# Performance work log

Measured on AMD Instinct MI355X. Metric: run time of the kernel, lower is better.

Reference implementation:

```python
import jax, jax.numpy as jnp
import numpy as np

DIM = 513          # SSP dimension (odd)
N_PARAM = (DIM - 1) // 2
BATCH = 131072


def setup_inputs() -> dict:
    key = jax.random.key(0)
    k1, k2 = jax.random.split(key)
    inputs = jax.random.normal(k1, (BATCH, 1), dtype=jnp.float32)
    # phis initialized uniform in (-pi+0.001, pi-0.001) like the torch module
    phis = jax.random.uniform(k2, (N_PARAM,), dtype=jnp.float32,
                              minval=-np.pi + 0.001, maxval=np.pi - 0.001)
    return {"inputs": inputs, "phis": phis}


def reference(inputs, phis):
    # uf is unit-modulus with conjugate-symmetric spectrum:
    #   uf[0] = 1, uf[1:h] = exp(i*phis), uf[-1:dim//2:-1] = conj(exp(i*phis))
    # so angle(uf) = [0, phis, -phis[::-1]] and uf**x = exp(i * x * angles).
    zero = jnp.zeros((1,), dtype=phis.dtype)
    angles = jnp.concatenate([zero, phis, -phis[::-1]])      # (dim,)
    # inputs: (B, 1) broadcasts against angles (dim,) -> (B, dim)
    spectrum = jnp.exp(1j * (inputs * angles[None, :]).astype(jnp.float32))
    out = jnp.fft.ifft(spectrum, axis=-1).real               # (B, dim)
    return out
```

## Files before the change

kernel.cpp:

```cpp
#include <hip/hip_runtime.h>


#define DIMN 513
#define KDIM 512
#define NPAD 544
#define NPAIRS 17
#define BM 128
#define INV_N (1.0f / 513.0f)

typedef __attribute__((ext_vector_type(8))) short short8;
typedef __attribute__((ext_vector_type(4))) float f32x4;
typedef __attribute__((ext_vector_type(4))) float f4;
typedef __attribute__((ext_vector_type(4), aligned(4))) float f4u;

__device__ __forceinline__ short bf16r(float f) {
  unsigned u = __float_as_uint(f);
  u += 0x7FFFu + ((u >> 16) & 1u);
  return (short)(u >> 16);
}

__global__ void ssp_genB(unsigned short* __restrict__ bt) {
  int idx = blockIdx.x * 256 + threadIdx.x;
  int n = idx >> 9;
  int k = idx & 511;
  int j = k & 255;
  unsigned prod = (unsigned)(j + 1) * (unsigned)n;
  unsigned m = prod % 513u;
  float ang = (float)m * (6.283185307179586f / 513.0f);
  float s, c;
  __sincosf(ang, &s, &c);
  float v = (k < 256) ? c * (2.0f / 513.0f) : -(s * (2.0f / 513.0f));
  unsigned chunk = (unsigned)n >> 5;
  unsigned w = ((unsigned)(n & 31) << 10) + ((unsigned)k << 1);
  unsigned phys = (chunk << 15) + (w ^ ((unsigned)(n & 7) << 4));
  bt[phys >> 1] = (unsigned short)bf16r(v);
}

__global__ __launch_bounds__(256, 2) void ssp_main(
    const float* __restrict__ x, const float* __restrict__ phis,
    const unsigned short* __restrict__ bt, float* __restrict__ out) {
  __shared__ __align__(16) unsigned char lds[65536];
  const int tid = threadIdx.x;
  const int w = tid >> 6;
  const int lane = tid & 63;
  const int r = lane & 15;
  const int q = lane >> 4;
  const long rowW = (long)blockIdx.x * BM + w * 32;

  const unsigned char* btb = (const unsigned char*)bt;

  {
    const unsigned char* src = btb + (w * 8) * 1024 + lane * 16;
    unsigned char* dst = &lds[(w * 8) * 1024];
#pragma unroll
    for (int i = 0; i < 8; ++i)
      __builtin_amdgcn_global_load_lds(
          (const __attribute__((address_space(1))) unsigned int*)(src + i * 1024),
          (__attribute__((address_space(3))) unsigned int*)(dst + i * 1024),
          16, 0, 0);
  }

  short8 afrag[2][16];
  const float x0 = x[rowW + r];
  const float x1 = x[rowW + 16 + r];
#pragma unroll
  for (int u = 0; u < 8; ++u) {
    const f4* pp4 = (const f4*)(phis + 32 * u + 8 * q);
    f4 plo = pp4[0];
    f4 phi4 = pp4[1];
#pragma unroll
    for (int e = 0; e < 8; ++e) {
      float ph = (e < 4) ? plo[e] : phi4[e - 4];
      float s0, c0, s1, c1;
      __sincosf(x0 * ph, &s0, &c0);
      __sincosf(x1 * ph, &s1, &c1);
      afrag[0][u][e]     = bf16r(c0);
      afrag[0][u + 8][e] = bf16r(s0);
      afrag[1][u][e]     = bf16r(c1);
      afrag[1][u + 8][e] = bf16r(s1);
    }
  }

  asm volatile("s_waitcnt vmcnt(0) lgkmcnt(0)" ::: "memory");
  __builtin_amdgcn_s_barrier();

  const int sw  = (r & 7) << 4;
  const int be0 = (r << 10)        + ((q << 4) ^ sw);
  const int bo0 = (r << 10)        + ((64 | (q << 4)) ^ sw);
  const int be1 = ((16 + r) << 10) + ((q << 4) ^ sw);
  const int bo1 = ((16 + r) << 10) + ((64 | (q << 4)) ^ sw);

  float* const o0 = out + (rowW + r) * DIMN;
  float* const o1 = out + (rowW + 16 + r) * DIMN;

  for (int p = 0; p < NPAIRS; ++p) {
    const int buf = (p & 1) * 32768;

    if (p + 1 < NPAIRS) {
      const unsigned char* src = btb + (p + 1) * 32768 + (w * 8) * 1024 + lane * 16;
      unsigned char* dst = &lds[((p + 1) & 1) * 32768 + (w * 8) * 1024];
#pragma unroll
      for (int i = 0; i < 8; ++i)
        __builtin_amdgcn_global_load_lds(
            (const __attribute__((address_space(1))) unsigned int*)(src + i * 1024),
            (__attribute__((address_space(3))) unsigned int*)(dst + i * 1024),
            16, 0, 0);
    }
    __builtin_amdgcn_sched_barrier(0);

    f32x4 acc00 = {0.f, 0.f, 0.f, 0.f};
    f32x4 acc01 = {0.f, 0.f, 0.f, 0.f};
    f32x4 acc10 = {0.f, 0.f, 0.f, 0.f};
    f32x4 acc11 = {0.f, 0.f, 0.f, 0.f};
#pragma unroll
    for (int t = 0; t < 16; ++t) {
      const int o0b = buf + ((t & 1) ? bo0 : be0) + (t >> 1) * 128;
      const int o1b = buf + ((t & 1) ? bo1 : be1) + (t >> 1) * 128;
      short8 b0 = *(const short8*)&lds[o0b];
      short8 b1 = *(const short8*)&lds[o1b];
      acc00 = __builtin_amdgcn_mfma_f32_16x16x32_bf16(b0, afrag[0][t], acc00, 0, 0, 0);
      acc10 = __builtin_amdgcn_mfma_f32_16x16x32_bf16(b0, afrag[1][t], acc10, 0, 0, 0);
      acc01 = __builtin_amdgcn_mfma_f32_16x16x32_bf16(b1, afrag[0][t], acc01, 0, 0, 0);
      acc11 = __builtin_amdgcn_mfma_f32_16x16x32_bf16(b1, afrag[1][t], acc11, 0, 0, 0);
    }

    const int nb = p * 32 + 4 * q;
    if (p < 16) {
      *(f4u*)(o0 + nb)      = acc00 + INV_N;
      *(f4u*)(o0 + nb + 16) = acc01 + INV_N;
      *(f4u*)(o1 + nb)      = acc10 + INV_N;
      *(f4u*)(o1 + nb + 16) = acc11 + INV_N;
    } else {
      if (q == 0) {
        o0[512] = acc00[0] + INV_N;
        o1[512] = acc10[0] + INV_N;
      }
    }
    __builtin_amdgcn_sched_barrier(0);

    asm volatile("s_waitcnt vmcnt(4)" ::: "memory");
    __builtin_amdgcn_s_barrier();
  }
}

extern "C" void kernel_launch(void* const* d_in, const int* in_sizes, int n_in,
                              void* d_out, int out_size, void* d_ws, size_t ws_size,
                              hipStream_t stream) {
  const float* x = (const float*)d_in[0];
  const float* phis = (const float*)d_in[1];
  float* out = (float*)d_out;
  unsigned short* bt = (unsigned short*)d_ws;

  ssp_genB<<<dim3(NPAD * KDIM / 256), dim3(256), 0, stream>>>(bt);
  ssp_main<<<dim3(131072 / BM), dim3(256), 0, stream>>>(x, phis, bt, out);
}
```

Measured before the change: 354.2 us.

## Split each block into eight waves of sixteen rows each

Doubles the threads per block to 512 so each wave computes 16 output rows instead of 32. This halves each wave's A-fragment and accumulator registers, and the B-tile prefetch is redistributed across eight waves. The aim is more resident waves to hide sincos, LDS and store latency. In exchange, each MFMA needs twice as many LDS reads of B, and the tighter launch bounds (512, 4) may squeeze the register budget enough to cause spills.

```diff
diff --git a/kernel.cpp b/kernel.cpp
--- a/kernel.cpp
+++ b/kernel.cpp
@@ -36,7 +36,7 @@
   bt[phys >> 1] = (unsigned short)bf16r(v);
 }
 
-__global__ __launch_bounds__(256, 2) void ssp_main(
+__global__ __launch_bounds__(512, 4) void ssp_main(
     const float* __restrict__ x, const float* __restrict__ phis,
     const unsigned short* __restrict__ bt, float* __restrict__ out) {
   __shared__ __align__(16) unsigned char lds[65536];
@@ -45,24 +45,23 @@
   const int lane = tid & 63;
   const int r = lane & 15;
   const int q = lane >> 4;
-  const long rowW = (long)blockIdx.x * BM + w * 32;
+  const long rowW = (long)blockIdx.x * BM + w * 16;
 
   const unsigned char* btb = (const unsigned char*)bt;
 
   {
-    const unsigned char* src = btb + (w * 8) * 1024 + lane * 16;
-    unsigned char* dst = &lds[(w * 8) * 1024];
 #pragma unroll
-    for (int i = 0; i < 8; ++i)
+    for (int i = 0; i < 4; ++i)
       __builtin_amdgcn_global_load_lds(
-          (const __attribute__((address_space(1))) unsigned int*)(src + i * 1024),
-          (__attribute__((address_space(3))) unsigned int*)(dst + i * 1024),
+          (const __attribute__((address_space(1))) unsigned int*)
+              (btb + w * 1024 + i * 8192 + lane * 16),
+          (__attribute__((address_space(3))) unsigned int*)
+              (&lds[w * 1024 + i * 8192]),
           16, 0, 0);
   }
 
-  short8 afrag[2][16];
+  short8 afrag[16];
   const float x0 = x[rowW + r];
-  const float x1 = x[rowW + 16 + r];
 #pragma unroll
   for (int u = 0; u < 8; ++u) {
     const f4* pp4 = (const f4*)(phis + 32 * u + 8 * q);
@@ -71,13 +70,10 @@
 #pragma unroll
     for (int e = 0; e < 8; ++e) {
       float ph = (e < 4) ? plo[e] : phi4[e - 4];
-      float s0, c0, s1, c1;
+      float s0, c0;
       __sincosf(x0 * ph, &s0, &c0);
-      __sincosf(x1 * ph, &s1, &c1);
-      afrag[0][u][e]     = bf16r(c0);
-      afrag[0][u + 8][e] = bf16r(s0);
-      afrag[1][u][e]     = bf16r(c1);
-      afrag[1][u + 8][e] = bf16r(s1);
+      afrag[u][e]     = bf16r(c0);
+      afrag[u + 8][e] = bf16r(s0);
     }
   }
 
@@ -91,54 +87,46 @@
   const int bo1 = ((16 + r) << 10) + ((64 | (q << 4)) ^ sw);
 
   float* const o0 = out + (rowW + r) * DIMN;
-  float* const o1 = out + (rowW + 16 + r) * DIMN;
 
   for (int p = 0; p < NPAIRS; ++p) {
     const int buf = (p & 1) * 32768;
 
     if (p + 1 < NPAIRS) {
-      const unsigned char* src = btb + (p + 1) * 32768 + (w * 8) * 1024 + lane * 16;
-      unsigned char* dst = &lds[((p + 1) & 1) * 32768 + (w * 8) * 1024];
+      const unsigned char* srcb = btb + (p + 1) * 32768;
+      const int dbuf = ((p + 1) & 1) * 32768;
 #pragma unroll
-      for (int i = 0; i < 8; ++i)
+      for (int i = 0; i < 4; ++i)
         __builtin_amdgcn_global_load_lds(
-            (const __attribute__((address_space(1))) unsigned int*)(src + i * 1024),
-            (__attribute__((address_space(3))) unsigned int*)(dst + i * 1024),
+            (const __attribute__((address_space(1))) unsigned int*)
+                (srcb + w * 1024 + i * 8192 + lane * 16),
+            (__attribute__((address_space(3))) unsigned int*)
+                (&lds[dbuf + w * 1024 + i * 8192]),
             16, 0, 0);
     }
     __builtin_amdgcn_sched_barrier(0);
 
-    f32x4 acc00 = {0.f, 0.f, 0.f, 0.f};
-    f32x4 acc01 = {0.f, 0.f, 0.f, 0.f};
-    f32x4 acc10 = {0.f, 0.f, 0.f, 0.f};
-    f32x4 acc11 = {0.f, 0.f, 0.f, 0.f};
+    f32x4 acc0 = {0.f, 0.f, 0.f, 0.f};
+    f32x4 acc1 = {0.f, 0.f, 0.f, 0.f};
 #pragma unroll
     for (int t = 0; t < 16; ++t) {
       const int o0b = buf + ((t & 1) ? bo0 : be0) + (t >> 1) * 128;
       const int o1b = buf + ((t & 1) ? bo1 : be1) + (t >> 1) * 128;
       short8 b0 = *(const short8*)&lds[o0b];
       short8 b1 = *(const short8*)&lds[o1b];
-      acc00 = __builtin_amdgcn_mfma_f32_16x16x32_bf16(b0, afrag[0][t], acc00, 0, 0, 0);
-      acc10 = __builtin_amdgcn_mfma_f32_16x16x32_bf16(b0, afrag[1][t], acc10, 0, 0, 0);
-      acc01 = __builtin_amdgcn_mfma_f32_16x16x32_bf16(b1, afrag[0][t], acc01, 0, 0, 0);
-      acc11 = __builtin_amdgcn_mfma_f32_16x16x32_bf16(b1, afrag[1][t], acc11, 0, 0, 0);
+      acc0 = __builtin_amdgcn_mfma_f32_16x16x32_bf16(b0, afrag[t], acc0, 0, 0, 0);
+      acc1 = __builtin_amdgcn_mfma_f32_16x16x32_bf16(b1, afrag[t], acc1, 0, 0, 0);
     }
 
     const int nb = p * 32 + 4 * q;
     if (p < 16) {
-      *(f4u*)(o0 + nb)      = acc00 + INV_N;
-      *(f4u*)(o0 + nb + 16) = acc01 + INV_N;
-      *(f4u*)(o1 + nb)      = acc10 + INV_N;
-      *(f4u*)(o1 + nb + 16) = acc11 + INV_N;
+      *(f4u*)(o0 + nb)      = acc0 + INV_N;
+      *(f4u*)(o0 + nb + 16) = acc1 + INV_N;
     } else {
-      if (q == 0) {
-        o0[512] = acc00[0] + INV_N;
-        o1[512] = acc10[0] + INV_N;
-      }
+      if (q == 0) o0[512] = acc0[0] + INV_N;
     }
     __builtin_amdgcn_sched_barrier(0);
 
-    asm volatile("s_waitcnt vmcnt(4)" ::: "memory");
+    asm volatile("s_waitcnt vmcnt(2)" ::: "memory");
     __builtin_amdgcn_s_barrier();
   }
 }
@@ -152,5 +140,5 @@
   unsigned short* bt = (unsigned short*)d_ws;
 
   ssp_genB<<<dim3(NPAD * KDIM / 256), dim3(256), 0, stream>>>(bt);
-  ssp_main<<<dim3(131072 / BM), dim3(256), 0, stream>>>(x, phis, bt, out);
+  ssp_main<<<dim3(131072 / BM), dim3(512), 0, stream>>>(x, phis, bt, out);
 }
```

New measurement: 357.5 us. About the same (+0.9%).
